# Optimization experiments

Measured on AMD Instinct MI355X. Metric: run time of the kernel, lower is better.

Reference implementation:

```python
import jax, jax.numpy as jnp
import numpy as np

EPS = 1e-5

def _bn_train(x, gamma, beta):
    # BatchNorm1d in training mode: biased batch stats over the edge dim
    mean = jnp.mean(x, axis=0)
    var = jnp.mean(jnp.square(x - mean), axis=0)
    return (x - mean) * (gamma / jnp.sqrt(var + EPS)) + beta

def setup_inputs() -> dict:
    key = jax.random.key(0)
    ks = jax.random.split(key, 12)
    E, F, G = 1000000, 64, 1024
    inp = {
        "src": jax.random.normal(ks[0], (E, F), jnp.float32),
        "dest": jax.random.normal(ks[1], (E, F), jnp.float32),
        "edge_attr": jax.random.normal(ks[2], (E, F), jnp.float32),
        "global_attr": jax.random.normal(ks[3], (G, F), jnp.float32),
        "batch": jax.random.randint(ks[4], (E,), 0, G, jnp.int64),
        # MLP params (torch Linear: y = x @ W.T + b); stored already transposed
        "W1": jax.random.normal(ks[5], (256, 64), jnp.float32) / np.sqrt(256.0),
        "b1": jnp.zeros((64,), jnp.float32),
        "W2": jax.random.normal(ks[6], (64, 64), jnp.float32) / 8.0,
        "b2": jnp.zeros((64,), jnp.float32),
        "W3": jax.random.normal(ks[7], (64, 64), jnp.float32) / 8.0,
        "b3": jnp.zeros((64,), jnp.float32),
        "g1": jnp.ones((64,), jnp.float32), "be1": jnp.zeros((64,), jnp.float32),
        "g2": jnp.ones((64,), jnp.float32), "be2": jnp.zeros((64,), jnp.float32),
        "g3": jnp.ones((64,), jnp.float32), "be3": jnp.zeros((64,), jnp.float32),
    }
    return inp

def reference(src, dest, edge_attr, global_attr, batch,
              W1, b1, W2, b2, W3, b3, g1, be1, g2, be2, g3, be3):
    # gather per-graph global attrs to edges, concat -> [E, 256]
    comb = jnp.concatenate([src, dest, edge_attr, global_attr[batch]], axis=1)
    out = _bn_train(jax.nn.relu(comb @ W1 + b1), g1, be1)
    out = _bn_train(jax.nn.relu(out @ W2 + b2), g2, be2)
    out = _bn_train(jax.nn.relu(out @ W3 + b3), g3, be3)
    # dropout p=0.0 -> identity
    return out
```

## Files before the change

### kernel.cpp

```cpp
#include <hip/hip_runtime.h>


typedef unsigned short u16;
typedef unsigned int u32;
using bf16x8 = __bf16 __attribute__((ext_vector_type(8)));
using f32x4  = float __attribute__((ext_vector_type(4)));
using u32x4  = u32 __attribute__((ext_vector_type(4)));

#define BN_EPS 1e-5f

__device__ __forceinline__ u16 f2bf(float f) {
    u32 u = __builtin_bit_cast(u32, f);
    u += 0x7fffu + ((u >> 16) & 1u);
    return (u16)(u >> 16);
}
__device__ __forceinline__ u32 pk2(float a, float b) {
    return (u32)f2bf(a) | ((u32)f2bf(b) << 16);
}

__global__ __launch_bounds__(256) void prep_kernel(const float* __restrict__ W1,
                                                   u16* __restrict__ w1f,
                                                   float* __restrict__ statsz) {
    int t = blockIdx.x * 256 + threadIdx.x;
    if (t < 16384) {
        int j = t & 7, lane = (t >> 3) & 63, ct = (t >> 9) & 3, s = (t >> 11) & 1, c = t >> 12;
        int m = lane & 15, quad = lane >> 4;
        int k = c * 64 + s * 32 + quad * 8 + j;
        int n = ct * 16 + m;
        w1f[t] = f2bf(W1[k * 64 + n]);
    }
    if (t < 384) statsz[t] = 0.0f;
}

__global__ __launch_bounds__(256) void gemm1_kernel(
    const float* __restrict__ src, const float* __restrict__ dst,
    const float* __restrict__ edg, const float* __restrict__ gat,
    const int* __restrict__ batch, const u16* __restrict__ w1f,
    const float* __restrict__ b1, u16* __restrict__ Y,
    float* __restrict__ stats, int tiles)
{
    __shared__ u16 sW[16384];
    __shared__ u16 sOut[4][1152];
    __shared__ float sSum[64], sSq[64];
    const int tid = threadIdx.x;
    {
        const u32x4* g = (const u32x4*)w1f;
        u32x4* l = (u32x4*)sW;
        #pragma unroll
        for (int i = 0; i < 8; i++) l[tid + i * 256] = g[tid + i * 256];
    }
    if (tid < 64) { sSum[tid] = 0.f; sSq[tid] = 0.f; }
    __syncthreads();

    const int wave = tid >> 6, lane = tid & 63;
    const int m = lane & 15, quad = lane >> 4;
    const u32x4* sWv = (const u32x4*)sW;
    u16* so = sOut[wave];

    float bias[4];
    #pragma unroll
    for (int ct = 0; ct < 4; ct++) bias[ct] = b1[ct * 16 + m];
    float ssum[4] = {0,0,0,0}, ssq[4] = {0,0,0,0};

    const int gs = gridDim.x;
    const int rowoff = wave * 16 + m;
    int t = blockIdx.x;
    int bi = (t < tiles) ? batch[(size_t)t * 64 + rowoff] : 0;

    for (; t < tiles; t += gs) {
        const size_t rbase = (size_t)t * 64 + wave * 16;
        float4 L[16];
        {
            const float* p0 = src + (rbase + m) * 64 + quad * 8;
            const float* p1 = dst + (rbase + m) * 64 + quad * 8;
            const float* p2 = edg + (rbase + m) * 64 + quad * 8;
            const float* p3 = gat + (size_t)bi * 64 + quad * 8;
            L[0]  = *(const float4*)(p0);      L[1]  = *(const float4*)(p0 + 4);
            L[2]  = *(const float4*)(p0 + 32); L[3]  = *(const float4*)(p0 + 36);
            L[4]  = *(const float4*)(p1);      L[5]  = *(const float4*)(p1 + 4);
            L[6]  = *(const float4*)(p1 + 32); L[7]  = *(const float4*)(p1 + 36);
            L[8]  = *(const float4*)(p2);      L[9]  = *(const float4*)(p2 + 4);
            L[10] = *(const float4*)(p2 + 32); L[11] = *(const float4*)(p2 + 36);
            L[12] = *(const float4*)(p3);      L[13] = *(const float4*)(p3 + 4);
            L[14] = *(const float4*)(p3 + 32); L[15] = *(const float4*)(p3 + 36);
        }
        int tn = t + gs;
        int bn = (tn < tiles) ? batch[(size_t)tn * 64 + rowoff] : 0;

        f32x4 acc[4] = {{0,0,0,0},{0,0,0,0},{0,0,0,0},{0,0,0,0}};
        #pragma unroll
        for (int c = 0; c < 4; c++) {
            #pragma unroll
            for (int s = 0; s < 2; s++) {
                float4 f0 = L[c * 4 + s * 2], f1 = L[c * 4 + s * 2 + 1];
                u32x4 av = { pk2(f0.x, f0.y), pk2(f0.z, f0.w),
                             pk2(f1.x, f1.y), pk2(f1.z, f1.w) };
                bf16x8 af = __builtin_bit_cast(bf16x8, av);
                #pragma unroll
                for (int ct = 0; ct < 4; ct++) {
                    bf16x8 bf = __builtin_bit_cast(bf16x8, sWv[((c * 2 + s) * 4 + ct) * 64 + lane]);
                    acc[ct] = __builtin_amdgcn_mfma_f32_16x16x32_bf16(af, bf, acc[ct], 0, 0, 0);
                }
            }
        }
        #pragma unroll
        for (int ct = 0; ct < 4; ct++) {
            #pragma unroll
            for (int r = 0; r < 4; r++) {
                float x = fmaxf(acc[ct][r] + bias[ct], 0.f);
                ssum[ct] += x; ssq[ct] = fmaf(x, x, ssq[ct]);
                so[(quad * 4 + r) * 72 + ct * 16 + m] = f2bf(x);
            }
        }
        __threadfence_block();
        {
            int row = lane >> 2, seg = lane & 3;
            const u16* rp = so + row * 72 + seg * 16;
            u32x4 v0 = *(const u32x4*)rp;
            u32x4 v1 = *(const u32x4*)(rp + 8);
            u16* yp = Y + (rbase + row) * 64 + seg * 16;
            *(u32x4*)yp = v0;
            *(u32x4*)(yp + 8) = v1;
        }
        bi = bn;
    }
    #pragma unroll
    for (int ct = 0; ct < 4; ct++) {
        float s = ssum[ct], q = ssq[ct];
        s += __shfl_xor(s, 16); s += __shfl_xor(s, 32);
        q += __shfl_xor(q, 16); q += __shfl_xor(q, 32);
        if (lane < 16) { atomicAdd(&sSum[ct * 16 + lane], s); atomicAdd(&sSq[ct * 16 + lane], q); }
    }
    __syncthreads();
    if (tid < 64) { atomicAdd(&stats[tid], sSum[tid]); atomicAdd(&stats[64 + tid], sSq[tid]); }
}

#define FOLD_PREAMBLE(STATS, G, BE, W, B)                                      \
    for (int i = tid; i < 1024; i += 256)                                      \
        ((float4*)sWf)[i] = ((const float4*)(W))[i];                           \
    if (tid < 64) {                                                            \
        float mean = (STATS)[tid] * invE;                                      \
        float var  = (STATS)[64 + tid] * invE - mean * mean;                   \
        float a = (G)[tid] / sqrtf(var + BN_EPS);                              \
        sAc[tid] = a; sCc[tid] = (BE)[tid] - mean * a;                         \
        sSum[tid] = 0.f; sSq[tid] = 0.f;                                       \
    }                                                                          \
    __syncthreads();                                                           \
    if (tid < 64) {                                                            \
        float bacc = (B)[tid];                                                 \
        for (int k = 0; k < 64; k++) bacc = fmaf(sCc[k], sWf[k * 64 + tid], bacc); \
        sBp[tid] = bacc;                                                       \
    }                                                                          \
    __syncthreads();                                                           \
    bf16x8 Bf[2][4];                                                           \
    float bias[4];                                                             \
    {                                                                          \
        _Pragma("unroll")                                                      \
        for (int s = 0; s < 2; s++) {                                          \
            _Pragma("unroll")                                                  \
            for (int ct = 0; ct < 4; ct++) {                                   \
                int n = ct * 16 + m;                                           \
                u32x4 wv;                                                      \
                _Pragma("unroll")                                              \
                for (int jj = 0; jj < 4; jj++) {                               \
                    int k = s * 32 + quad * 8 + jj * 2;                        \
                    wv[jj] = pk2(sAc[k] * sWf[k * 64 + n],                     \
                                 sAc[k + 1] * sWf[(k + 1) * 64 + n]);          \
                }                                                              \
                Bf[s][ct] = __builtin_bit_cast(bf16x8, wv);                    \
            }                                                                  \
        }                                                                      \
        _Pragma("unroll")                                                      \
        for (int ct = 0; ct < 4; ct++) bias[ct] = sBp[ct * 16 + m];            \
    }

__global__ __launch_bounds__(256) void gemm_mid_kernel(
    const u16* __restrict__ X, const float* __restrict__ W, const float* __restrict__ b,
    const float* __restrict__ stats_in, float invE,
    const float* __restrict__ g, const float* __restrict__ be,
    u16* __restrict__ Y, float* __restrict__ stats_out, int tiles)
{
    __shared__ float sWf[4096];
    __shared__ float sAc[64], sCc[64], sBp[64];
    __shared__ float sSum[64], sSq[64];
    __shared__ u16 sOut[4][1152];
    const int tid = threadIdx.x;
    const int wave = tid >> 6, lane = tid & 63;
    const int m = lane & 15, quad = lane >> 4;

    FOLD_PREAMBLE(stats_in, g, be, W, b)

    float ssum[4] = {0,0,0,0}, ssq[4] = {0,0,0,0};
    u16* so = sOut[wave];
    const int nw = gridDim.x * 4;
    for (int t = blockIdx.x * 4 + wave; t < tiles; t += nw) {
        u32x4 Xf[8];
        const u16* xb = X + (size_t)t * 4096 + m * 64 + quad * 8;
        #pragma unroll
        for (int u = 0; u < 4; u++) {
            Xf[u * 2]     = *(const u32x4*)(xb + u * 1024);
            Xf[u * 2 + 1] = *(const u32x4*)(xb + u * 1024 + 32);
        }
        #pragma unroll
        for (int u = 0; u < 4; u++) {
            f32x4 acc[4] = {{0,0,0,0},{0,0,0,0},{0,0,0,0},{0,0,0,0}};
            #pragma unroll
            for (int s = 0; s < 2; s++) {
                bf16x8 af = __builtin_bit_cast(bf16x8, Xf[u * 2 + s]);
                #pragma unroll
                for (int ct = 0; ct < 4; ct++)
                    acc[ct] = __builtin_amdgcn_mfma_f32_16x16x32_bf16(af, Bf[s][ct], acc[ct], 0, 0, 0);
            }
            #pragma unroll
            for (int ct = 0; ct < 4; ct++) {
                #pragma unroll
                for (int r = 0; r < 4; r++) {
                    float x = fmaxf(acc[ct][r] + bias[ct], 0.f);
                    ssum[ct] += x; ssq[ct] = fmaf(x, x, ssq[ct]);
                    so[(quad * 4 + r) * 72 + ct * 16 + m] = f2bf(x);
                }
            }
            __threadfence_block();
            int row = lane >> 2, seg = lane & 3;
            const u16* rp = so + row * 72 + seg * 16;
            u32x4 v0 = *(const u32x4*)rp;
            u32x4 v1 = *(const u32x4*)(rp + 8);
            u16* yp = Y + (size_t)t * 4096 + (u * 16 + row) * 64 + seg * 16;
            *(u32x4*)yp = v0;
            *(u32x4*)(yp + 8) = v1;
        }
    }
    #pragma unroll
    for (int ct = 0; ct < 4; ct++) {
        float s = ssum[ct], q = ssq[ct];
        s += __shfl_xor(s, 16); s += __shfl_xor(s, 32);
        q += __shfl_xor(q, 16); q += __shfl_xor(q, 32);
        if (lane < 16) { atomicAdd(&sSum[ct * 16 + lane], s); atomicAdd(&sSq[ct * 16 + lane], q); }
    }
    __syncthreads();
    if (tid < 64) { atomicAdd(&stats_out[tid], sSum[tid]); atomicAdd(&stats_out[64 + tid], sSq[tid]); }
}

__global__ __launch_bounds__(256) void gemm_stats_kernel(
    const u16* __restrict__ X, const float* __restrict__ W, const float* __restrict__ b,
    const float* __restrict__ stats_in, float invE,
    const float* __restrict__ g, const float* __restrict__ be,
    float* __restrict__ stats_out, int tiles)
{
    __shared__ float sWf[4096];
    __shared__ float sAc[64], sCc[64], sBp[64];
    __shared__ float sSum[64], sSq[64];
    const int tid = threadIdx.x;
    const int wave = tid >> 6, lane = tid & 63;
    const int m = lane & 15, quad = lane >> 4;

    FOLD_PREAMBLE(stats_in, g, be, W, b)

    float ssum[4] = {0,0,0,0}, ssq[4] = {0,0,0,0};
    const int nw = gridDim.x * 4;
    for (int t = blockIdx.x * 4 + wave; t < tiles; t += nw) {
        u32x4 Xf[8];
        const u16* xb = X + (size_t)t * 4096 + m * 64 + quad * 8;
        #pragma unroll
        for (int u = 0; u < 4; u++) {
            Xf[u * 2]     = *(const u32x4*)(xb + u * 1024);
            Xf[u * 2 + 1] = *(const u32x4*)(xb + u * 1024 + 32);
        }
        #pragma unroll
        for (int u = 0; u < 4; u++) {
            f32x4 acc[4] = {{0,0,0,0},{0,0,0,0},{0,0,0,0},{0,0,0,0}};
            #pragma unroll
            for (int s = 0; s < 2; s++) {
                bf16x8 af = __builtin_bit_cast(bf16x8, Xf[u * 2 + s]);
                #pragma unroll
                for (int ct = 0; ct < 4; ct++)
                    acc[ct] = __builtin_amdgcn_mfma_f32_16x16x32_bf16(af, Bf[s][ct], acc[ct], 0, 0, 0);
            }
            #pragma unroll
            for (int ct = 0; ct < 4; ct++) {
                #pragma unroll
                for (int r = 0; r < 4; r++) {
                    float x = fmaxf(acc[ct][r] + bias[ct], 0.f);
                    ssum[ct] += x; ssq[ct] = fmaf(x, x, ssq[ct]);
                }
            }
        }
    }
    #pragma unroll
    for (int ct = 0; ct < 4; ct++) {
        float s = ssum[ct], q = ssq[ct];
        s += __shfl_xor(s, 16); s += __shfl_xor(s, 32);
        q += __shfl_xor(q, 16); q += __shfl_xor(q, 32);
        if (lane < 16) { atomicAdd(&sSum[ct * 16 + lane], s); atomicAdd(&sSq[ct * 16 + lane], q); }
    }
    __syncthreads();
    if (tid < 64) { atomicAdd(&stats_out[tid], sSum[tid]); atomicAdd(&stats_out[64 + tid], sSq[tid]); }
}

__global__ __launch_bounds__(256) void gemm_out_kernel(
    const u16* __restrict__ X, const float* __restrict__ W, const float* __restrict__ b,
    const float* __restrict__ stats_in, float invE,
    const float* __restrict__ g, const float* __restrict__ be,
    const float* __restrict__ stats3, const float* __restrict__ g3,
    const float* __restrict__ be3, float* __restrict__ out, int tiles)
{
    __shared__ float sWf[4096];
    __shared__ float sAc[64], sCc[64], sBp[64];
    __shared__ float sSum[64], sSq[64];
    __shared__ float sA3[64], sC3[64];
    __shared__ float sOutF[4][1088];
    const int tid = threadIdx.x;
    const int wave = tid >> 6, lane = tid & 63;
    const int m = lane & 15, quad = lane >> 4;

    if (tid < 64) {
        float mean = stats3[tid] * invE;
        float var  = stats3[64 + tid] * invE - mean * mean;
        float a = g3[tid] / sqrtf(var + BN_EPS);
        sA3[tid] = a; sC3[tid] = be3[tid] - mean * a;
    }
    FOLD_PREAMBLE(stats_in, g, be, W, b)

    float a3r[4], c3r[4];
    #pragma unroll
    for (int ct = 0; ct < 4; ct++) { a3r[ct] = sA3[ct * 16 + m]; c3r[ct] = sC3[ct * 16 + m]; }

    float* sof = sOutF[wave];
    const int nw = gridDim.x * 4;
    for (int t = blockIdx.x * 4 + wave; t < tiles; t += nw) {
        u32x4 Xf[8];
        const u16* xb = X + (size_t)t * 4096 + m * 64 + quad * 8;
        #pragma unroll
        for (int u = 0; u < 4; u++) {
            Xf[u * 2]     = *(const u32x4*)(xb + u * 1024);
            Xf[u * 2 + 1] = *(const u32x4*)(xb + u * 1024 + 32);
        }
        #pragma unroll
        for (int u = 0; u < 4; u++) {
            f32x4 acc[4] = {{0,0,0,0},{0,0,0,0},{0,0,0,0},{0,0,0,0}};
            #pragma unroll
            for (int s = 0; s < 2; s++) {
                bf16x8 af = __builtin_bit_cast(bf16x8, Xf[u * 2 + s]);
                #pragma unroll
                for (int ct = 0; ct < 4; ct++)
                    acc[ct] = __builtin_amdgcn_mfma_f32_16x16x32_bf16(af, Bf[s][ct], acc[ct], 0, 0, 0);
            }
            #pragma unroll
            for (int ct = 0; ct < 4; ct++) {
                #pragma unroll
                for (int r = 0; r < 4; r++) {
                    float x = fmaxf(acc[ct][r] + bias[ct], 0.f);
                    sof[(quad * 4 + r) * 68 + ct * 16 + m] = fmaf(a3r[ct], x, c3r[ct]);
                }
            }
            __threadfence_block();
            int row = lane >> 2, seg = lane & 3;
            const float* rp = sof + row * 68 + seg * 16;
            float4 v0 = *(const float4*)rp;
            float4 v1 = *(const float4*)(rp + 4);
            float4 v2 = *(const float4*)(rp + 8);
            float4 v3 = *(const float4*)(rp + 12);
            float* op = out + ((size_t)t * 64 + u * 16 + row) * 64 + seg * 16;
            *(float4*)op       = v0;
            *(float4*)(op + 4) = v1;
            *(float4*)(op + 8) = v2;
            *(float4*)(op + 12) = v3;
        }
    }
    (void)sSum; (void)sSq;
}

extern "C" void kernel_launch(void* const* d_in, const int* in_sizes, int n_in,
                              void* d_out, int out_size, void* d_ws, size_t ws_size,
                              hipStream_t stream)
{
    const float* src  = (const float*)d_in[0];
    const float* dst  = (const float*)d_in[1];
    const float* edg  = (const float*)d_in[2];
    const float* gat  = (const float*)d_in[3];
    const int*   batch= (const int*)d_in[4];
    const float* W1 = (const float*)d_in[5];
    const float* b1 = (const float*)d_in[6];
    const float* W2 = (const float*)d_in[7];
    const float* b2 = (const float*)d_in[8];
    const float* W3 = (const float*)d_in[9];
    const float* b3 = (const float*)d_in[10];
    const float* g1 = (const float*)d_in[11];
    const float* be1= (const float*)d_in[12];
    const float* g2 = (const float*)d_in[13];
    const float* be2= (const float*)d_in[14];
    const float* g3 = (const float*)d_in[15];
    const float* be3= (const float*)d_in[16];

    const int E = in_sizes[0] / 64;
    const int tiles = E / 64;
    const float invE = 1.0f / (float)E;

    char* ws = (char*)d_ws;
    u16*   w1f = (u16*)(ws + 0);
    float* st1 = (float*)(ws + 49152);
    float* st2 = st1 + 128;
    float* st3 = st1 + 256;

    const size_t OFF_H = 65536;
    const size_t HSZ = (size_t)E * 128;
    u16 *h1, *h2;
    if (ws_size >= OFF_H + 2 * HSZ) {
        h1 = (u16*)(ws + OFF_H); h2 = (u16*)(ws + OFF_H + HSZ);
    } else {
        h1 = (u16*)d_out; h2 = (u16*)(ws + OFF_H);
    }

    prep_kernel<<<64, 256, 0, stream>>>(W1, w1f, st1);
    gemm1_kernel<<<1536, 256, 0, stream>>>(src, dst, edg, gat, batch, w1f, b1, h1, st1, tiles);
    gemm_mid_kernel<<<1024, 256, 0, stream>>>(h1, W2, b2, st1, invE, g1, be1, h2, st2, tiles);
    gemm_stats_kernel<<<1024, 256, 0, stream>>>(h2, W3, b3, st2, invE, g2, be2, st3, tiles);
    gemm_out_kernel<<<1024, 256, 0, stream>>>(h2, W3, b3, st2, invE, g2, be2, st3, g3, be3,
                                              (float*)d_out, tiles);
}
```

Before: 938.2 us.

## Swap MFMA operands so each lane writes its own output row directly

The MFMA operands are swapped, with weights as A and activations as B. Each lane's accumulator therefore holds 4 consecutive output features of a single row, so results can be stored straight to global memory as packed 8-byte bf16 or 16-byte fp32 vectors. This removes the per-wave LDS staging buffer, the block fence, and the re-read that previously transposed results before coalesced stores. Stats reduction moves to within-16-lane shuffles, and grid sizes are raised to use the freed LDS. The trade-off is less contiguous global stores per instruction and more shuffle and atomic work at the end.

```diff
diff --git a/kernel.cpp b/kernel.cpp
--- a/kernel.cpp
+++ b/kernel.cpp
@@ -5,6 +5,7 @@
 typedef unsigned int u32;
 using bf16x8 = __bf16 __attribute__((ext_vector_type(8)));
 using f32x4  = float __attribute__((ext_vector_type(4)));
+using u32x2  = u32 __attribute__((ext_vector_type(2)));
 using u32x4  = u32 __attribute__((ext_vector_type(4)));
 
 #define BN_EPS 1e-5f
@@ -23,10 +24,10 @@
                                                    float* __restrict__ statsz) {
     int t = blockIdx.x * 256 + threadIdx.x;
     if (t < 16384) {
-        int j = t & 7, lane = (t >> 3) & 63, ct = (t >> 9) & 3, s = (t >> 11) & 1, c = t >> 12;
+        int j = t & 7, lane = (t >> 3) & 63, fa = (t >> 9) & 3, s = (t >> 11) & 1, c = t >> 12;
         int m = lane & 15, quad = lane >> 4;
         int k = c * 64 + s * 32 + quad * 8 + j;
-        int n = ct * 16 + m;
+        int n = fa * 16 + m;
         w1f[t] = f2bf(W1[k * 64 + n]);
     }
     if (t < 384) statsz[t] = 0.0f;
@@ -40,7 +41,6 @@
     float* __restrict__ stats, int tiles)
 {
     __shared__ u16 sW[16384];
-    __shared__ u16 sOut[4][1152];
     __shared__ float sSum[64], sSq[64];
     const int tid = threadIdx.x;
     {
@@ -55,12 +55,12 @@
     const int wave = tid >> 6, lane = tid & 63;
     const int m = lane & 15, quad = lane >> 4;
     const u32x4* sWv = (const u32x4*)sW;
-    u16* so = sOut[wave];
-
-    float bias[4];
+
+    f32x4 bias4[4];
     #pragma unroll
-    for (int ct = 0; ct < 4; ct++) bias[ct] = b1[ct * 16 + m];
-    float ssum[4] = {0,0,0,0}, ssq[4] = {0,0,0,0};
+    for (int fa = 0; fa < 4; fa++) bias4[fa] = *(const f32x4*)(b1 + fa * 16 + quad * 4);
+    f32x4 ssum4[4] = {{0,0,0,0},{0,0,0,0},{0,0,0,0},{0,0,0,0}};
+    f32x4 ssq4[4]  = {{0,0,0,0},{0,0,0,0},{0,0,0,0},{0,0,0,0}};
 
     const int gs = gridDim.x;
     const int rowoff = wave * 16 + m;
@@ -95,41 +95,40 @@
                 float4 f0 = L[c * 4 + s * 2], f1 = L[c * 4 + s * 2 + 1];
                 u32x4 av = { pk2(f0.x, f0.y), pk2(f0.z, f0.w),
                              pk2(f1.x, f1.y), pk2(f1.z, f1.w) };
-                bf16x8 af = __builtin_bit_cast(bf16x8, av);
-                #pragma unroll
-                for (int ct = 0; ct < 4; ct++) {
-                    bf16x8 bf = __builtin_bit_cast(bf16x8, sWv[((c * 2 + s) * 4 + ct) * 64 + lane]);
-                    acc[ct] = __builtin_amdgcn_mfma_f32_16x16x32_bf16(af, bf, acc[ct], 0, 0, 0);
+                bf16x8 xv = __builtin_bit_cast(bf16x8, av);
+                #pragma unroll
+                for (int fa = 0; fa < 4; fa++) {
+                    bf16x8 wf = __builtin_bit_cast(bf16x8, sWv[((c * 2 + s) * 4 + fa) * 64 + lane]);
+                    acc[fa] = __builtin_amdgcn_mfma_f32_16x16x32_bf16(wf, xv, acc[fa], 0, 0, 0);
                 }
             }
         }
-        #pragma unroll
-        for (int ct = 0; ct < 4; ct++) {
-            #pragma unroll
-            for (int r = 0; r < 4; r++) {
-                float x = fmaxf(acc[ct][r] + bias[ct], 0.f);
-                ssum[ct] += x; ssq[ct] = fmaf(x, x, ssq[ct]);
-                so[(quad * 4 + r) * 72 + ct * 16 + m] = f2bf(x);
-            }
-        }
-        __threadfence_block();
-        {
-            int row = lane >> 2, seg = lane & 3;
-            const u16* rp = so + row * 72 + seg * 16;
-            u32x4 v0 = *(const u32x4*)rp;
-            u32x4 v1 = *(const u32x4*)(rp + 8);
-            u16* yp = Y + (rbase + row) * 64 + seg * 16;
-            *(u32x4*)yp = v0;
-            *(u32x4*)(yp + 8) = v1;
+        u16* yrow = Y + (rbase + m) * 64;
+        #pragma unroll
+        for (int fa = 0; fa < 4; fa++) {
+            f32x4 x;
+            #pragma unroll
+            for (int r = 0; r < 4; r++) x[r] = fmaxf(acc[fa][r] + bias4[fa][r], 0.f);
+            ssum4[fa] += x;
+            #pragma unroll
+            for (int r = 0; r < 4; r++) ssq4[fa][r] = fmaf(x[r], x[r], ssq4[fa][r]);
+            u32x2 pv = { pk2(x[0], x[1]), pk2(x[2], x[3]) };
+            *(u32x2*)(yrow + fa * 16 + quad * 4) = pv;
         }
         bi = bn;
     }
     #pragma unroll
-    for (int ct = 0; ct < 4; ct++) {
-        float s = ssum[ct], q = ssq[ct];
-        s += __shfl_xor(s, 16); s += __shfl_xor(s, 32);
-        q += __shfl_xor(q, 16); q += __shfl_xor(q, 32);
-        if (lane < 16) { atomicAdd(&sSum[ct * 16 + lane], s); atomicAdd(&sSq[ct * 16 + lane], q); }
+    for (int fa = 0; fa < 4; fa++) {
+        #pragma unroll
+        for (int r = 0; r < 4; r++) {
+            float s = ssum4[fa][r], q = ssq4[fa][r];
+            s += __shfl_xor(s, 1); s += __shfl_xor(s, 2); s += __shfl_xor(s, 4); s += __shfl_xor(s, 8);
+            q += __shfl_xor(q, 1); q += __shfl_xor(q, 2); q += __shfl_xor(q, 4); q += __shfl_xor(q, 8);
+            if (m == 0) {
+                atomicAdd(&sSum[fa * 16 + quad * 4 + r], s);
+                atomicAdd(&sSq [fa * 16 + quad * 4 + r], q);
+            }
+        }
     }
     __syncthreads();
     if (tid < 64) { atomicAdd(&stats[tid], sSum[tid]); atomicAdd(&stats[64 + tid], sSq[tid]); }
@@ -152,14 +151,14 @@
         sBp[tid] = bacc;                                                       \
     }                                                                          \
     __syncthreads();                                                           \
-    bf16x8 Bf[2][4];                                                           \
-    float bias[4];                                                             \
+    bf16x8 Wf[2][4];                                                           \
+    f32x4 bias4[4];                                                            \
     {                                                                          \
         _Pragma("unroll")                                                      \
         for (int s = 0; s < 2; s++) {                                          \
             _Pragma("unroll")                                                  \
-            for (int ct = 0; ct < 4; ct++) {                                   \
-                int n = ct * 16 + m;                                           \
+            for (int fa = 0; fa < 4; fa++) {                                   \
+                int n = fa * 16 + m;                                           \
                 u32x4 wv;                                                      \
                 _Pragma("unroll")                                              \
                 for (int jj = 0; jj < 4; jj++) {                               \
@@ -167,11 +166,12 @@
                     wv[jj] = pk2(sAc[k] * sWf[k * 64 + n],                     \
                                  sAc[k + 1] * sWf[(k + 1) * 64 + n]);          \
                 }                                                              \
-                Bf[s][ct] = __builtin_bit_cast(bf16x8, wv);                    \
+                Wf[s][fa] = __builtin_bit_cast(bf16x8, wv);                    \
             }                                                                  \
         }                                                                      \
         _Pragma("unroll")                                                      \
-        for (int ct = 0; ct < 4; ct++) bias[ct] = sBp[ct * 16 + m];            \
+        for (int fa = 0; fa < 4; fa++)                                         \
+            bias4[fa] = *(const f32x4*)&sBp[fa * 16 + quad * 4];               \
     }
 
 __global__ __launch_bounds__(256) void gemm_mid_kernel(
@@ -183,15 +183,14 @@
     __shared__ float sWf[4096];
     __shared__ float sAc[64], sCc[64], sBp[64];
     __shared__ float sSum[64], sSq[64];
-    __shared__ u16 sOut[4][1152];
     const int tid = threadIdx.x;
     const int wave = tid >> 6, lane = tid & 63;
     const int m = lane & 15, quad = lane >> 4;
 
     FOLD_PREAMBLE(stats_in, g, be, W, b)
 
-    float ssum[4] = {0,0,0,0}, ssq[4] = {0,0,0,0};
-    u16* so = sOut[wave];
+    f32x4 ssum4[4] = {{0,0,0,0},{0,0,0,0},{0,0,0,0},{0,0,0,0}};
+    f32x4 ssq4[4]  = {{0,0,0,0},{0,0,0,0},{0,0,0,0},{0,0,0,0}};
     const int nw = gridDim.x * 4;
     for (int t = blockIdx.x * 4 + wave; t < tiles; t += nw) {
         u32x4 Xf[8];
@@ -206,36 +205,37 @@
             f32x4 acc[4] = {{0,0,0,0},{0,0,0,0},{0,0,0,0},{0,0,0,0}};
             #pragma unroll
             for (int s = 0; s < 2; s++) {
-                bf16x8 af = __builtin_bit_cast(bf16x8, Xf[u * 2 + s]);
-                #pragma unroll
-                for (int ct = 0; ct < 4; ct++)
-                    acc[ct] = __builtin_amdgcn_mfma_f32_16x16x32_bf16(af, Bf[s][ct], acc[ct], 0, 0, 0);
-            }
-            #pragma unroll
-            for (int ct = 0; ct < 4; ct++) {
-                #pragma unroll
-                for (int r = 0; r < 4; r++) {
-                    float x = fmaxf(acc[ct][r] + bias[ct], 0.f);
-                    ssum[ct] += x; ssq[ct] = fmaf(x, x, ssq[ct]);
-                    so[(quad * 4 + r) * 72 + ct * 16 + m] = f2bf(x);
-                }
-            }
-            __threadfence_block();
-            int row = lane >> 2, seg = lane & 3;
-            const u16* rp = so + row * 72 + seg * 16;
-            u32x4 v0 = *(const u32x4*)rp;
-            u32x4 v1 = *(const u32x4*)(rp + 8);
-            u16* yp = Y + (size_t)t * 4096 + (u * 16 + row) * 64 + seg * 16;
-            *(u32x4*)yp = v0;
-            *(u32x4*)(yp + 8) = v1;
+                bf16x8 xv = __builtin_bit_cast(bf16x8, Xf[u * 2 + s]);
+                #pragma unroll
+                for (int fa = 0; fa < 4; fa++)
+                    acc[fa] = __builtin_amdgcn_mfma_f32_16x16x32_bf16(Wf[s][fa], xv, acc[fa], 0, 0, 0);
+            }
+            u16* yrow = Y + (size_t)t * 4096 + (u * 16 + m) * 64;
+            #pragma unroll
+            for (int fa = 0; fa < 4; fa++) {
+                f32x4 x;
+                #pragma unroll
+                for (int r = 0; r < 4; r++) x[r] = fmaxf(acc[fa][r] + bias4[fa][r], 0.f);
+                ssum4[fa] += x;
+                #pragma unroll
+                for (int r = 0; r < 4; r++) ssq4[fa][r] = fmaf(x[r], x[r], ssq4[fa][r]);
+                u32x2 pv = { pk2(x[0], x[1]), pk2(x[2], x[3]) };
+                *(u32x2*)(yrow + fa * 16 + quad * 4) = pv;
+            }
         }
     }
     #pragma unroll
-    for (int ct = 0; ct < 4; ct++) {
-        float s = ssum[ct], q = ssq[ct];
-        s += __shfl_xor(s, 16); s += __shfl_xor(s, 32);
-        q += __shfl_xor(q, 16); q += __shfl_xor(q, 32);
-        if (lane < 16) { atomicAdd(&sSum[ct * 16 + lane], s); atomicAdd(&sSq[ct * 16 + lane], q); }
+    for (int fa = 0; fa < 4; fa++) {
+        #pragma unroll
+        for (int r = 0; r < 4; r++) {
+            float s = ssum4[fa][r], q = ssq4[fa][r];
+            s += __shfl_xor(s, 1); s += __shfl_xor(s, 2); s += __shfl_xor(s, 4); s += __shfl_xor(s, 8);
+            q += __shfl_xor(q, 1); q += __shfl_xor(q, 2); q += __shfl_xor(q, 4); q += __shfl_xor(q, 8);
+            if (m == 0) {
+                atomicAdd(&sSum[fa * 16 + quad * 4 + r], s);
+                atomicAdd(&sSq [fa * 16 + quad * 4 + r], q);
+            }
+        }
     }
     __syncthreads();
     if (tid < 64) { atomicAdd(&stats_out[tid], sSum[tid]); atomicAdd(&stats_out[64 + tid], sSq[tid]); }
@@ -256,7 +256,8 @@
 
     FOLD_PREAMBLE(stats_in, g, be, W, b)
 
-    float ssum[4] = {0,0,0,0}, ssq[4] = {0,0,0,0};
+    f32x4 ssum4[4] = {{0,0,0,0},{0,0,0,0},{0,0,0,0},{0,0,0,0}};
+    f32x4 ssq4[4]  = {{0,0,0,0},{0,0,0,0},{0,0,0,0},{0,0,0,0}};
     const int nw = gridDim.x * 4;
     for (int t = blockIdx.x * 4 + wave; t < tiles; t += nw) {
         u32x4 Xf[8];
@@ -271,27 +272,34 @@
             f32x4 acc[4] = {{0,0,0,0},{0,0,0,0},{0,0,0,0},{0,0,0,0}};
             #pragma unroll
             for (int s = 0; s < 2; s++) {
-                bf16x8 af = __builtin_bit_cast(bf16x8, Xf[u * 2 + s]);
-                #pragma unroll
-                for (int ct = 0; ct < 4; ct++)
-                    acc[ct] = __builtin_amdgcn_mfma_f32_16x16x32_bf16(af, Bf[s][ct], acc[ct], 0, 0, 0);
-            }
-            #pragma unroll
-            for (int ct = 0; ct < 4; ct++) {
-                #pragma unroll
-                for (int r = 0; r < 4; r++) {
-                    float x = fmaxf(acc[ct][r] + bias[ct], 0.f);
-                    ssum[ct] += x; ssq[ct] = fmaf(x, x, ssq[ct]);
-                }
+                bf16x8 xv = __builtin_bit_cast(bf16x8, Xf[u * 2 + s]);
+                #pragma unroll
+                for (int fa = 0; fa < 4; fa++)
+                    acc[fa] = __builtin_amdgcn_mfma_f32_16x16x32_bf16(Wf[s][fa], xv, acc[fa], 0, 0, 0);
+            }
+            #pragma unroll
+            for (int fa = 0; fa < 4; fa++) {
+                f32x4 x;
+                #pragma unroll
+                for (int r = 0; r < 4; r++) x[r] = fmaxf(acc[fa][r] + bias4[fa][r], 0.f);
+                ssum4[fa] += x;
+                #pragma unroll
+                for (int r = 0; r < 4; r++) ssq4[fa][r] = fmaf(x[r], x[r], ssq4[fa][r]);
             }
         }
     }
     #pragma unroll
-    for (int ct = 0; ct < 4; ct++) {
-        float s = ssum[ct], q = ssq[ct];
-        s += __shfl_xor(s, 16); s += __shfl_xor(s, 32);
-        q += __shfl_xor(q, 16); q += __shfl_xor(q, 32);
-        if (lane < 16) { atomicAdd(&sSum[ct * 16 + lane], s); atomicAdd(&sSq[ct * 16 + lane], q); }
+    for (int fa = 0; fa < 4; fa++) {
+        #pragma unroll
+        for (int r = 0; r < 4; r++) {
+            float s = ssum4[fa][r], q = ssq4[fa][r];
+            s += __shfl_xor(s, 1); s += __shfl_xor(s, 2); s += __shfl_xor(s, 4); s += __shfl_xor(s, 8);
+            q += __shfl_xor(q, 1); q += __shfl_xor(q, 2); q += __shfl_xor(q, 4); q += __shfl_xor(q, 8);
+            if (m == 0) {
+                atomicAdd(&sSum[fa * 16 + quad * 4 + r], s);
+                atomicAdd(&sSq [fa * 16 + quad * 4 + r], q);
+            }
+        }
     }
     __syncthreads();
     if (tid < 64) { atomicAdd(&stats_out[tid], sSum[tid]); atomicAdd(&stats_out[64 + tid], sSq[tid]); }
@@ -308,7 +316,6 @@
     __shared__ float sAc[64], sCc[64], sBp[64];
     __shared__ float sSum[64], sSq[64];
     __shared__ float sA3[64], sC3[64];
-    __shared__ float sOutF[4][1088];
     const int tid = threadIdx.x;
     const int wave = tid >> 6, lane = tid & 63;
     const int m = lane & 15, quad = lane >> 4;
@@ -321,11 +328,13 @@
     }
     FOLD_PREAMBLE(stats_in, g, be, W, b)
 
-    float a3r[4], c3r[4];
+    f32x4 a34[4], c34[4];
     #pragma unroll
-    for (int ct = 0; ct < 4; ct++) { a3r[ct] = sA3[ct * 16 + m]; c3r[ct] = sC3[ct * 16 + m]; }
-
-    float* sof = sOutF[wave];
+    for (int fa = 0; fa < 4; fa++) {
+        a34[fa] = *(const f32x4*)&sA3[fa * 16 + quad * 4];
+        c34[fa] = *(const f32x4*)&sC3[fa * 16 + quad * 4];
+    }
+
     const int nw = gridDim.x * 4;
     for (int t = blockIdx.x * 4 + wave; t < tiles; t += nw) {
         u32x4 Xf[8];
@@ -340,31 +349,22 @@
             f32x4 acc[4] = {{0,0,0,0},{0,0,0,0},{0,0,0,0},{0,0,0,0}};
             #pragma unroll
             for (int s = 0; s < 2; s++) {
-                bf16x8 af = __builtin_bit_cast(bf16x8, Xf[u * 2 + s]);
-                #pragma unroll
-                for (int ct = 0; ct < 4; ct++)
-                    acc[ct] = __builtin_amdgcn_mfma_f32_16x16x32_bf16(af, Bf[s][ct], acc[ct], 0, 0, 0);
-            }
-            #pragma unroll
-            for (int ct = 0; ct < 4; ct++) {
+                bf16x8 xv = __builtin_bit_cast(bf16x8, Xf[u * 2 + s]);
+                #pragma unroll
+                for (int fa = 0; fa < 4; fa++)
+                    acc[fa] = __builtin_amdgcn_mfma_f32_16x16x32_bf16(Wf[s][fa], xv, acc[fa], 0, 0, 0);
+            }
+            float* orow = out + ((size_t)t * 64 + u * 16 + m) * 64;
+            #pragma unroll
+            for (int fa = 0; fa < 4; fa++) {
+                f32x4 o;
                 #pragma unroll
                 for (int r = 0; r < 4; r++) {
-                    float x = fmaxf(acc[ct][r] + bias[ct], 0.f);
-                    sof[(quad * 4 + r) * 68 + ct * 16 + m] = fmaf(a3r[ct], x, c3r[ct]);
+                    float x = fmaxf(acc[fa][r] + bias4[fa][r], 0.f);
+                    o[r] = fmaf(a34[fa][r], x, c34[fa][r]);
                 }
-            }
-            __threadfence_block();
-            int row = lane >> 2, seg = lane & 3;
-            const float* rp = sof + row * 68 + seg * 16;
-            float4 v0 = *(const float4*)rp;
-            float4 v1 = *(const float4*)(rp + 4);
-            float4 v2 = *(const float4*)(rp + 8);
-            float4 v3 = *(const float4*)(rp + 12);
-            float* op = out + ((size_t)t * 64 + u * 16 + row) * 64 + seg * 16;
-            *(float4*)op       = v0;
-            *(float4*)(op + 4) = v1;
-            *(float4*)(op + 8) = v2;
-            *(float4*)(op + 12) = v3;
+                *(f32x4*)(orow + fa * 16 + quad * 4) = o;
+            }
         }
     }
     (void)sSum; (void)sSq;
@@ -412,9 +412,9 @@
     }
 
     prep_kernel<<<64, 256, 0, stream>>>(W1, w1f, st1);
-    gemm1_kernel<<<1536, 256, 0, stream>>>(src, dst, edg, gat, batch, w1f, b1, h1, st1, tiles);
-    gemm_mid_kernel<<<1024, 256, 0, stream>>>(h1, W2, b2, st1, invE, g1, be1, h2, st2, tiles);
-    gemm_stats_kernel<<<1024, 256, 0, stream>>>(h2, W3, b3, st2, invE, g2, be2, st3, tiles);
-    gemm_out_kernel<<<1024, 256, 0, stream>>>(h2, W3, b3, st2, invE, g2, be2, st3, g3, be3,
+    gemm1_kernel<<<2048, 256, 0, stream>>>(src, dst, edg, gat, batch, w1f, b1, h1, st1, tiles);
+    gemm_mid_kernel<<<1536, 256, 0, stream>>>(h1, W2, b2, st1, invE, g1, be1, h2, st2, tiles);
+    gemm_stats_kernel<<<1536, 256, 0, stream>>>(h2, W3, b3, st2, invE, g2, be2, st3, tiles);
+    gemm_out_kernel<<<1536, 256, 0, stream>>>(h2, W3, b3, st2, invE, g2, be2, st3, g3, be3,
                                               (float*)d_out, tiles);
 }
```

Result: slower. 994.7 us (+6.0%).
